# Optimization experiments

Hardware: AMD Instinct MI355X
Metric: run time of the kernel (lower is better)

The kernel has to match this reference:

```python
import jax, jax.numpy as jnp
import numpy as np

B, T, S, E = 32, 32, 8, 512
H, D, FF, NL = 8, 64, 2048, 4
AEMB, NACT = 64, 18
L = T * S            # qlen = 256
MEM = 256
KLEN = L + MEM       # 512


def _ln(x, g, b, eps=1e-5):
    m = jnp.mean(x, -1, keepdims=True)
    v = jnp.mean(jnp.square(x - m), -1, keepdims=True)
    return (x - m) * jax.lax.rsqrt(v + eps) * g + b


def _rel_shift(bd):
    # bd: [qlen, klen, B, H] -- TransformerXL rel-shift trick
    q, k, b, h = bd.shape
    bd = jnp.pad(bd, ((0, 0), (1, 0), (0, 0), (0, 0)))
    return bd.reshape(k + 1, q, b, h)[1:].reshape(q, k, b, h)


def setup_inputs() -> dict:
    key = jax.random.key(0)
    ks = jax.random.split(key, 20)
    s = 0.02  # weight init scale
    x = jax.random.normal(ks[0], (B, T, S, E), jnp.float32)
    action = jax.random.randint(ks[1], (B, T), 0, NACT, dtype=jnp.int32)
    i = jnp.arange(L)[:, None]
    j = jnp.arange(KLEN)[None, :]
    attn_mask = j > (i + MEM)                      # True = masked (causal w/ memory)
    positions = jnp.arange(KLEN - 1, -1, -1, dtype=jnp.int32)  # TXL descending positions
    mems = jax.random.normal(ks[2], (NL, MEM, B, E), jnp.float32) * 0.1
    return {
        'x': x, 'action': action, 'attn_mask': attn_mask, 'positions': positions,
        'mems': mems,
        'act_emb': jax.random.normal(ks[3], (NACT, AEMB), jnp.float32) * s,
        'stem_w1': jax.random.normal(ks[4], (E + AEMB, E), jnp.float32) * s,
        'stem_ln1_g': jnp.ones((E,), jnp.float32), 'stem_ln1_b': jnp.zeros((E,), jnp.float32),
        'stem_w2': jax.random.normal(ks[5], (E, E), jnp.float32) * s,
        'stem_ln2_g': jnp.ones((E,), jnp.float32), 'stem_ln2_b': jnp.zeros((E,), jnp.float32),
        'lnf_g': jnp.ones((E,), jnp.float32), 'lnf_b': jnp.zeros((E,), jnp.float32),
        'u_bias': jax.random.normal(ks[6], (H, D), jnp.float32) * s,
        'v_bias': jax.random.normal(ks[7], (H, D), jnp.float32) * s,
        'Wqkv': jax.random.normal(ks[8], (NL, E, 3 * H * D), jnp.float32) * s,
        'Wr': jax.random.normal(ks[9], (NL, E, H * D), jnp.float32) * s,
        'Wo': jax.random.normal(ks[10], (NL, H * D, E), jnp.float32) * s,
        'ln1_g': jnp.ones((NL, E), jnp.float32), 'ln1_b': jnp.zeros((NL, E), jnp.float32),
        'W1': jax.random.normal(ks[11], (NL, E, FF), jnp.float32) * s,
        'b1': jnp.zeros((NL, FF), jnp.float32),
        'W2': jax.random.normal(ks[12], (NL, FF, E), jnp.float32) * s,
        'b2': jnp.zeros((NL, E), jnp.float32),
        'ln2_g': jnp.ones((NL, E), jnp.float32), 'ln2_b': jnp.zeros((NL, E), jnp.float32),
    }


def reference(x, action, attn_mask, positions, mems, act_emb,
              stem_w1, stem_ln1_g, stem_ln1_b, stem_w2, stem_ln2_g, stem_ln2_b,
              lnf_g, lnf_b, u_bias, v_bias, Wqkv, Wr, Wo,
              ln1_g, ln1_b, W1, b1, W2, b2, ln2_g, ln2_b):
    Bv, Tv, Sv, Ev = x.shape
    Hh, Dd = u_bias.shape
    qlen = Tv * Sv
    # --- stem (StateMixer, concat type) ---
    xs = x.reshape(Bv, qlen, Ev).transpose(1, 0, 2)                # [L,B,E] time-major
    a = act_emb[action]                                            # [B,T,AEMB]
    a = jnp.repeat(a, Sv, axis=1).transpose(1, 0, 2)               # [L,B,AEMB]
    h = jnp.concatenate([xs, a], -1) @ stem_w1
    h = jax.nn.relu(_ln(h, stem_ln1_g, stem_ln1_b))
    h = _ln(h @ stem_w2, stem_ln2_g, stem_ln2_b)
    feats = _ln(h, lnf_g, lnf_b, eps=1e-6)
    # --- sinusoidal positional encoding of relative positions ---
    pf = positions.astype(jnp.float32)
    inv = 1.0 / (10000.0 ** (jnp.arange(0, Ev, 2, dtype=jnp.float32) / Ev))
    ang = pf[:, None] * inv[None, :]
    pos_emb = jnp.concatenate([jnp.sin(ang), jnp.cos(ang)], -1)    # [KLEN,E]
    scale = 1.0 / np.sqrt(Dd)
    out = feats
    for l in range(Wqkv.shape[0]):
        cat = jnp.concatenate([mems[l], out], 0)                   # [klen,B,E]
        klen = cat.shape[0]
        q, k, v = jnp.split(cat @ Wqkv[l], 3, -1)
        q = q[-qlen:].reshape(qlen, Bv, Hh, Dd)
        k = k.reshape(klen, Bv, Hh, Dd)
        v = v.reshape(klen, Bv, Hh, Dd)
        r = (pos_emb @ Wr[l]).reshape(klen, Hh, Dd)
        AC = jnp.einsum('ibhd,jbhd->ijbh', q + u_bias, k)
        BD = _rel_shift(jnp.einsum('ibhd,jhd->ijbh', q + v_bias, r))
        score = (AC + BD) * scale
        score = jnp.where(attn_mask[:, :, None, None], jnp.float32(-1e30), score)
        attn = jax.nn.softmax(score, axis=1)
        ao = jnp.einsum('ijbh,jbhd->ibhd', attn, v).reshape(qlen, Bv, Hh * Dd) @ Wo[l]
        h1 = _ln(out + ao, ln1_g[l], ln1_b[l])
        ff = jax.nn.relu(h1 @ W1[l] + b1[l]) @ W2[l] + b2[l]
        out = _ln(h1 + ff, ln2_g[l], ln2_b[l])
    return out.transpose(1, 0, 2).reshape(Bv, Tv, Sv, Ev)
```

## Files before the change

### kernel.cpp

```cpp
#include <hip/hip_runtime.h>


typedef __attribute__((ext_vector_type(8))) short bf8_t;
typedef __attribute__((ext_vector_type(4))) float f4_t;
typedef __attribute__((ext_vector_type(16))) float fx16;

__device__ __forceinline__ ushort f2bf(float f) {
    uint u = __float_as_uint(f);
    u += 0x7FFFu + ((u >> 16) & 1u);
    return (ushort)(u >> 16);
}
__device__ __forceinline__ float b2f(ushort h) {
    return __uint_as_float(((uint)h) << 16);
}
__device__ __forceinline__ void gload16(const void* g, void* l) {
    __builtin_amdgcn_global_load_lds((const __attribute__((address_space(1))) void*)g,
                                     (__attribute__((address_space(3))) void*)l, 16, 0, 0);
}

__device__ __forceinline__ void mma32_step(const ushort* __restrict__ As,
                                           const ushort* __restrict__ Bs,
                                           int rowA0, int colB0,
                                           int l31, int hi, fx16 acc[2][2])
{
#pragma unroll
    for (int kk = 0; kk < 4; ++kk) {
        bf8_t av[2], bv[2];
#pragma unroll
        for (int i = 0; i < 2; ++i) {
            const int row = rowA0 + i * 32 + l31;
            const int ch = (kk * 2 + hi) ^ (row & 7);
            av[i] = *(const bf8_t*)(As + row * 64 + ch * 8);
        }
#pragma unroll
        for (int j = 0; j < 2; ++j) {
            const int row = colB0 + j * 32 + l31;
            const int ch = (kk * 2 + hi) ^ (row & 7);
            bv[j] = *(const bf8_t*)(Bs + row * 64 + ch * 8);
        }
#pragma unroll
        for (int i = 0; i < 2; ++i)
#pragma unroll
            for (int j = 0; j < 2; ++j)
                acc[i][j] = __builtin_amdgcn_mfma_f32_32x32x16_bf16(av[i], bv[j], acc[i][j], 0, 0, 0);
    }
}

template<bool BIAS, bool RELU, bool OUTBF>
__global__ __launch_bounds__(256)
void gemm_bf(const ushort* __restrict__ A, int lda,
             const ushort* __restrict__ Bt, int ldb,
             const float* __restrict__ bias,
             void* __restrict__ Cp, int ldc,
             int M, int N, int K)
{
    __shared__ __align__(16) ushort sh[17408];
    ushort* As = sh;
    ushort* Bs = sh + 8192;
    const int t = threadIdx.x;
    const int w = t >> 6, lane = t & 63;
    const int wr = w >> 1, wc = w & 1;
    const int l31 = lane & 31, hi = lane >> 5;
    const int m0 = blockIdx.y * 128, n0 = blockIdx.x * 128;

    const int srow = w * 8 + (lane >> 3);
    const int gchunk = (lane & 7) ^ (srow & 7);
    const ushort* Ag = A + (size_t)(m0 + srow) * lda + gchunk * 8;
    const ushort* Bg = Bt + (size_t)(n0 + srow) * ldb + gchunk * 8;
    ushort* Asw = As + w * 512;
    ushort* Bsw = Bs + w * 512;

    fx16 acc[2][2];
#pragma unroll
    for (int i = 0; i < 2; ++i)
#pragma unroll
        for (int j = 0; j < 2; ++j)
#pragma unroll
            for (int r = 0; r < 16; ++r) acc[i][j][r] = 0.f;

    for (int k0 = 0; k0 < K; k0 += 64) {
#pragma unroll
        for (int c = 0; c < 4; ++c) {
            gload16(Ag + (size_t)c * 32 * lda, Asw + c * 2048);
            gload16(Bg + (size_t)c * 32 * ldb, Bsw + c * 2048);
        }
        Ag += 64; Bg += 64;
        __syncthreads();
        mma32_step(As, Bs, wr * 64, wc * 64, l31, hi, acc);
        __syncthreads();
    }
    const int crow0 = wr * 64, ccol0 = wc * 64;
    if (OUTBF) {
        ushort* Cs = sh;
#pragma unroll
        for (int i = 0; i < 2; ++i)
#pragma unroll
            for (int j = 0; j < 2; ++j) {
                const int colb = ccol0 + j * 32 + l31;
                float bb = BIAS ? bias[n0 + colb] : 0.f;
                fx16 v = acc[i][j];
#pragma unroll
                for (int r = 0; r < 16; ++r) {
                    float o = v[r] + bb;
                    if (RELU) o = fmaxf(o, 0.f);
                    const int rw = crow0 + i * 32 + (r & 3) + 8 * (r >> 2) + 4 * hi;
                    Cs[rw * 136 + colb] = f2bf(o);
                }
            }
        __syncthreads();
        const int orow = t >> 1, oc0 = (t & 1) * 64;
        ushort* dst = (ushort*)Cp + (size_t)(m0 + orow) * ldc + n0 + oc0;
#pragma unroll
        for (int u = 0; u < 8; ++u)
            *(bf8_t*)(dst + u * 8) = *(const bf8_t*)(Cs + orow * 136 + oc0 + u * 8);
    } else {
        float* C = (float*)Cp;
#pragma unroll
        for (int i = 0; i < 2; ++i)
#pragma unroll
            for (int j = 0; j < 2; ++j) {
                const int colb = n0 + ccol0 + j * 32 + l31;
                float bb = BIAS ? bias[colb] : 0.f;
                fx16 v = acc[i][j];
#pragma unroll
                for (int r = 0; r < 16; ++r) {
                    float o = v[r] + bb;
                    if (RELU) o = fmaxf(o, 0.f);
                    const int rw = crow0 + i * 32 + (r & 3) + 8 * (r >> 2) + 4 * hi;
                    C[(size_t)(m0 + rw) * ldc + colb] = o;
                }
            }
    }
}

__global__ __launch_bounds__(256)
void gemm_qkv(const ushort* __restrict__ A, const ushort* __restrict__ Bt,
              ushort* __restrict__ qout, ushort* __restrict__ kvout)
{
    __shared__ __align__(16) ushort sh[17408];
    ushort* As = sh;
    ushort* Bs = sh + 8192;
    const int t = threadIdx.x;
    const int w = t >> 6, lane = t & 63;
    const int wr = w >> 1, wc = w & 1;
    const int l31 = lane & 31, hi = lane >> 5;
    const int m0 = blockIdx.y * 128, n0 = blockIdx.x * 128;

    const int srow = w * 8 + (lane >> 3);
    const int gchunk = (lane & 7) ^ (srow & 7);
    const ushort* Ag = A + (size_t)(m0 + srow) * 512 + gchunk * 8;
    const ushort* Bg = Bt + (size_t)(n0 + srow) * 512 + gchunk * 8;
    ushort* Asw = As + w * 512;
    ushort* Bsw = Bs + w * 512;

    fx16 acc[2][2];
#pragma unroll
    for (int i = 0; i < 2; ++i)
#pragma unroll
        for (int j = 0; j < 2; ++j)
#pragma unroll
            for (int r = 0; r < 16; ++r) acc[i][j][r] = 0.f;

    for (int k0 = 0; k0 < 512; k0 += 64) {
#pragma unroll
        for (int c = 0; c < 4; ++c) {
            gload16(Ag + (size_t)c * 32 * 512, Asw + c * 2048);
            gload16(Bg + (size_t)c * 32 * 512, Bsw + c * 2048);
        }
        Ag += 64; Bg += 64;
        __syncthreads();
        mma32_step(As, Bs, wr * 64, wc * 64, l31, hi, acc);
        __syncthreads();
    }
    const int crow0 = wr * 64, ccol0 = wc * 64;
    ushort* Cs = sh;
#pragma unroll
    for (int i = 0; i < 2; ++i)
#pragma unroll
        for (int j = 0; j < 2; ++j) {
            const int colb = ccol0 + j * 32 + l31;
            fx16 v = acc[i][j];
#pragma unroll
            for (int r = 0; r < 16; ++r) {
                const int rw = crow0 + i * 32 + (r & 3) + 8 * (r >> 2) + 4 * hi;
                Cs[rw * 136 + colb] = f2bf(v[r]);
            }
        }
    __syncthreads();
    ushort* base; size_t ldc2;
    if (n0 < 512) { base = qout + n0; ldc2 = 512; }
    else          { base = kvout + (size_t)8192 * 1024 + (n0 - 512); ldc2 = 1024; }
    const int orow = t >> 1, oc0 = (t & 1) * 64;
    ushort* dst = base + (size_t)(m0 + orow) * ldc2 + oc0;
#pragma unroll
    for (int u = 0; u < 8; ++u)
        *(bf8_t*)(dst + u * 8) = *(const bf8_t*)(Cs + orow * 136 + oc0 + u * 8);
}

template<bool BIAS>
__global__ __launch_bounds__(256)
void gemm_sk(const ushort* __restrict__ A, int lda,
             const ushort* __restrict__ Bt, int ldb,
             const float* __restrict__ bias,
             float* __restrict__ C0, float* __restrict__ C1, int ldc, int KH)
{
    __shared__ __align__(16) ushort sh[16384];
    ushort* As = sh;
    ushort* Bs = sh + 8192;
    const int t = threadIdx.x;
    const int w = t >> 6, lane = t & 63;
    const int wr = w >> 1, wc = w & 1;
    const int l31 = lane & 31, hi = lane >> 5;
    const int m0 = blockIdx.y * 128, n0 = blockIdx.x * 128;
    const int z = blockIdx.z;
    A += (size_t)z * KH; Bt += (size_t)z * KH;
    float* C = z ? C1 : C0;

    const int srow = w * 8 + (lane >> 3);
    const int gchunk = (lane & 7) ^ (srow & 7);
    const ushort* Ag = A + (size_t)(m0 + srow) * lda + gchunk * 8;
    const ushort* Bg = Bt + (size_t)(n0 + srow) * ldb + gchunk * 8;
    ushort* Asw = As + w * 512;
    ushort* Bsw = Bs + w * 512;

    fx16 acc[2][2];
#pragma unroll
    for (int i = 0; i < 2; ++i)
#pragma unroll
        for (int j = 0; j < 2; ++j)
#pragma unroll
            for (int r = 0; r < 16; ++r) acc[i][j][r] = 0.f;

    for (int k0 = 0; k0 < KH; k0 += 64) {
#pragma unroll
        for (int c = 0; c < 4; ++c) {
            gload16(Ag + (size_t)c * 32 * lda, Asw + c * 2048);
            gload16(Bg + (size_t)c * 32 * ldb, Bsw + c * 2048);
        }
        Ag += 64; Bg += 64;
        __syncthreads();
        mma32_step(As, Bs, wr * 64, wc * 64, l31, hi, acc);
        __syncthreads();
    }
    const int crow0 = wr * 64, ccol0 = wc * 64;
#pragma unroll
    for (int i = 0; i < 2; ++i)
#pragma unroll
        for (int j = 0; j < 2; ++j) {
            const int colb = n0 + ccol0 + j * 32 + l31;
            float bb = (BIAS && z == 0) ? bias[colb] : 0.f;
            fx16 v = acc[i][j];
#pragma unroll
            for (int r = 0; r < 16; ++r) {
                const int rw = crow0 + i * 32 + (r & 3) + 8 * (r >> 2) + 4 * hi;
                C[(size_t)(m0 + rw) * ldc + colb] = v[r] + bb;
            }
        }
}

template<int RMODE, bool TROUT>
__global__ __launch_bounds__(256)
void ln_k(const float* __restrict__ X, const float* __restrict__ X2,
          const void* __restrict__ Rp,
          const float* __restrict__ g, const float* __restrict__ bt,
          float* __restrict__ Yf, ushort* __restrict__ Yb,
          float eps, int do_relu)
{
    const int row  = blockIdx.x * 4 + (threadIdx.x >> 6);
    const int lane = threadIdx.x & 63;
    const float* xp = X + (size_t)row * 512 + lane * 8;
    float4 x0 = *(const float4*)xp, x1 = *(const float4*)(xp + 4);
    float v[8] = {x0.x, x0.y, x0.z, x0.w, x1.x, x1.y, x1.z, x1.w};
    if (RMODE == 3 || RMODE == 4) {
        const float* p2 = X2 + (size_t)row * 512 + lane * 8;
        float4 a0 = *(const float4*)p2, a1 = *(const float4*)(p2 + 4);
        v[0] += a0.x; v[1] += a0.y; v[2] += a0.z; v[3] += a0.w;
        v[4] += a1.x; v[5] += a1.y; v[6] += a1.z; v[7] += a1.w;
    }
    if (RMODE == 1 || RMODE == 4) {
        const float* rp = (const float*)Rp + (size_t)row * 512 + lane * 8;
        float4 r0 = *(const float4*)rp, r1 = *(const float4*)(rp + 4);
        v[0] += r0.x; v[1] += r0.y; v[2] += r0.z; v[3] += r0.w;
        v[4] += r1.x; v[5] += r1.y; v[6] += r1.z; v[7] += r1.w;
    } else if (RMODE == 2 || RMODE == 3) {
        const ushort* rp = (const ushort*)Rp + (size_t)row * 512 + lane * 8;
        ushort4 r0 = *(const ushort4*)rp, r1 = *(const ushort4*)(rp + 4);
        v[0] += b2f(r0.x); v[1] += b2f(r0.y); v[2] += b2f(r0.z); v[3] += b2f(r0.w);
        v[4] += b2f(r1.x); v[5] += b2f(r1.y); v[6] += b2f(r1.z); v[7] += b2f(r1.w);
    }
    float s = 0.f;
#pragma unroll
    for (int i = 0; i < 8; ++i) s += v[i];
#pragma unroll
    for (int m = 1; m < 64; m <<= 1) s += __shfl_xor(s, m);
    float mean = s * (1.f / 512.f);
    float q = 0.f;
#pragma unroll
    for (int i = 0; i < 8; ++i) { float d = v[i] - mean; q = fmaf(d, d, q); }
#pragma unroll
    for (int m = 1; m < 64; m <<= 1) q += __shfl_xor(q, m);
    float rstd = rsqrtf(q * (1.f / 512.f) + eps);
    float4 g0 = *(const float4*)(g + lane * 8), g1 = *(const float4*)(g + lane * 8 + 4);
    float4 c0 = *(const float4*)(bt + lane * 8), c1 = *(const float4*)(bt + lane * 8 + 4);
    float gv[8] = {g0.x, g0.y, g0.z, g0.w, g1.x, g1.y, g1.z, g1.w};
    float bv[8] = {c0.x, c0.y, c0.z, c0.w, c1.x, c1.y, c1.z, c1.w};
    float o[8];
#pragma unroll
    for (int i = 0; i < 8; ++i) {
        o[i] = (v[i] - mean) * rstd * gv[i] + bv[i];
        if (do_relu) o[i] = fmaxf(o[i], 0.f);
    }
    if (Yf) {
        float* yp;
        if (TROUT) {
            const int bq = row & 31, lq = row >> 5;
            yp = Yf + ((size_t)bq * 256 + lq) * 512 + lane * 8;
        } else {
            yp = Yf + (size_t)row * 512 + lane * 8;
        }
        *(float4*)yp       = make_float4(o[0], o[1], o[2], o[3]);
        *(float4*)(yp + 4) = make_float4(o[4], o[5], o[6], o[7]);
    }
    if (Yb) {
        ushort* yp = Yb + (size_t)row * 512 + lane * 8;
        ushort4 w0, w1;
        w0.x = f2bf(o[0]); w0.y = f2bf(o[1]); w0.z = f2bf(o[2]); w0.w = f2bf(o[3]);
        w1.x = f2bf(o[4]); w1.y = f2bf(o[5]); w1.z = f2bf(o[6]); w1.w = f2bf(o[7]);
        *(ushort4*)yp       = w0;
        *(ushort4*)(yp + 4) = w1;
    }
}

__global__ __launch_bounds__(256)
void ln_stem2(const float* __restrict__ X,
              const float* __restrict__ g1, const float* __restrict__ b1,
              const float* __restrict__ g2, const float* __restrict__ b2,
              float* __restrict__ Yf, ushort* __restrict__ Yb)
{
    const int row  = blockIdx.x * 4 + (threadIdx.x >> 6);
    const int lane = threadIdx.x & 63;
    const float* xp = X + (size_t)row * 512 + lane * 8;
    float4 x0 = *(const float4*)xp, x1 = *(const float4*)(xp + 4);
    float v[8] = {x0.x, x0.y, x0.z, x0.w, x1.x, x1.y, x1.z, x1.w};
    float s = 0.f;
#pragma unroll
    for (int i = 0; i < 8; ++i) s += v[i];
#pragma unroll
    for (int m = 1; m < 64; m <<= 1) s += __shfl_xor(s, m);
    float mean = s * (1.f / 512.f);
    float q = 0.f;
#pragma unroll
    for (int i = 0; i < 8; ++i) { float d = v[i] - mean; q = fmaf(d, d, q); }
#pragma unroll
    for (int m = 1; m < 64; m <<= 1) q += __shfl_xor(q, m);
    float rstd = rsqrtf(q * (1.f / 512.f) + 1e-5f);
#pragma unroll
    for (int i = 0; i < 8; ++i)
        v[i] = (v[i] - mean) * rstd * g1[lane * 8 + i] + b1[lane * 8 + i];
    s = 0.f;
#pragma unroll
    for (int i = 0; i < 8; ++i) s += v[i];
#pragma unroll
    for (int m = 1; m < 64; m <<= 1) s += __shfl_xor(s, m);
    mean = s * (1.f / 512.f);
    q = 0.f;
#pragma unroll
    for (int i = 0; i < 8; ++i) { float d = v[i] - mean; q = fmaf(d, d, q); }
#pragma unroll
    for (int m = 1; m < 64; m <<= 1) q += __shfl_xor(q, m);
    rstd = rsqrtf(q * (1.f / 512.f) + 1e-6f);
    float o[8];
#pragma unroll
    for (int i = 0; i < 8; ++i)
        o[i] = (v[i] - mean) * rstd * g2[lane * 8 + i] + b2[lane * 8 + i];
    float* yp = Yf + (size_t)row * 512 + lane * 8;
    *(float4*)yp       = make_float4(o[0], o[1], o[2], o[3]);
    *(float4*)(yp + 4) = make_float4(o[4], o[5], o[6], o[7]);
    ushort* yb = Yb + (size_t)row * 512 + lane * 8;
    ushort4 w0, w1;
    w0.x = f2bf(o[0]); w0.y = f2bf(o[1]); w0.z = f2bf(o[2]); w0.w = f2bf(o[3]);
    w1.x = f2bf(o[4]); w1.y = f2bf(o[5]); w1.z = f2bf(o[6]); w1.w = f2bf(o[7]);
    *(ushort4*)yb       = w0;
    *(ushort4*)(yb + 4) = w1;
}

__global__ __launch_bounds__(256)
void wtrans(const float* __restrict__ in, ushort* __restrict__ out, int K, int N)
{
    __shared__ float tl[32][33];
    const size_t bo = (size_t)blockIdx.z * K * N;
    in += bo; out += bo;
    const int k0 = blockIdx.y * 32, n0 = blockIdx.x * 32;
    const int tx = threadIdx.x & 31, ty = threadIdx.x >> 5;
    for (int i = ty; i < 32; i += 8) tl[i][tx] = in[(size_t)(k0 + i) * N + n0 + tx];
    __syncthreads();
    for (int i = ty; i < 32; i += 8) out[(size_t)(n0 + i) * K + k0 + tx] = f2bf(tl[tx][i]);
}

__global__ void convk(const float* __restrict__ in, ushort* __restrict__ out)
{
    int i = (blockIdx.x * 256 + threadIdx.x) * 4;
    float4 v = *(const float4*)(in + i);
    ushort4 o;
    o.x = f2bf(v.x); o.y = f2bf(v.y); o.z = f2bf(v.z); o.w = f2bf(v.w);
    *(ushort4*)(out + i) = o;
}

__global__ void build_xcat(const float* __restrict__ x, const int* __restrict__ action,
                           const float* __restrict__ act_emb, ushort* __restrict__ xcat)
{
    int idx = blockIdx.x * 256 + threadIdx.x;
    int n = idx / 576, e = idx - n * 576;
    int l = n >> 5, b = n & 31;
    float v;
    if (e < 512) v = x[((size_t)b * 256 + l) * 512 + e];
    else         v = act_emb[action[b * 32 + (l >> 3)] * 64 + (e - 512)];
    xcat[idx] = f2bf(v);
}

__global__ void build_posemb(ushort* __restrict__ pe)
{
    int idx = blockIdx.x * 256 + threadIdx.x;
    int j = idx >> 9, c = idx & 511;
    float pf = (float)(511 - j);
    int i2 = (c < 256) ? c : c - 256;
    float inv = expf(-(float)i2 * 0.03597789207803197f);
    float ang = pf * inv;
    pe[idx] = f2bf((c < 256) ? sinf(ang) : cosf(ang));
}

__global__ __launch_bounds__(512)
void attn_mfma(const ushort* __restrict__ q,
               const ushort* __restrict__ kv,
               const ushort* __restrict__ rb,
               const float* __restrict__ ub, const float* __restrict__ vb,
               ushort* __restrict__ ao)
{
    __shared__ __align__(16) ushort Ks[64][72];
    __shared__ __align__(16) ushort Vs[64][72];
    __shared__ __align__(16) ushort Rs[192][72];
    __shared__ __align__(16) ushort Ps[8][16][72];
    const int t = threadIdx.x;
    const int wv = t >> 6, lane = t & 63;
    const int lc = lane & 15, lr = lane >> 4;
    const int bh = (int)blockIdx.x >> 1, ihalf = blockIdx.x & 1;
    const int b = bh >> 3, h = bh & 7;
    const int i0 = ihalf << 7;
    const int iw = i0 + wv * 16;

    bf8_t au[2], aw[2];
#pragma unroll
    for (int kk = 0; kk < 2; ++kk) {
        const ushort* qp = q + ((size_t)(iw + lc) * 32 + b) * 512 + h * 64 + kk * 32 + lr * 8;
        bf8_t q8 = *(const bf8_t*)qp;
        const float* up = ub + h * 64 + kk * 32 + lr * 8;
        const float* vp = vb + h * 64 + kk * 32 + lr * 8;
#pragma unroll
        for (int e = 0; e < 8; ++e) {
            float qf = b2f((ushort)q8[e]);
            au[kk][e] = (short)f2bf(qf + up[e]);
            aw[kk][e] = (short)f2bf(qf + vp[e]);
        }
    }

    const int jl = t >> 3, d0 = (t & 7) * 8;
    const int vrow = ((t >> 3) & 7) * 8 + wv;

    f4_t o[4];
#pragma unroll
    for (int d = 0; d < 4; ++d) o[d] = (f4_t){0.f, 0.f, 0.f, 0.f};
    float mrun[4] = {-3.0e38f, -3.0e38f, -3.0e38f, -3.0e38f};
    float lrun[4] = {0.f, 0.f, 0.f, 0.f};

    {
        *(bf8_t*)&Ks[jl][d0] = *(const bf8_t*)(kv + ((size_t)jl * 32 + b) * 1024 + h * 64 + d0);
        bf8_t vv = *(const bf8_t*)(kv + ((size_t)vrow * 32 + b) * 1024 + 512 + h * 64 + d0);
#pragma unroll
        for (int e = 0; e < 8; ++e) Vs[d0 + e][vrow] = (ushort)vv[e];
        const int rbase0 = 128 - i0;
#pragma unroll
        for (int p = 0; p < 3; ++p) {
            const int jr = min(rbase0 + p * 64 + jl, 511);
            *(bf8_t*)&Rs[p * 64 + jl][d0] = *(const bf8_t*)(rb + (size_t)jr * 512 + h * 64 + d0);
        }
    }
    __syncthreads();

    const int njt = ihalf ? 8 : 6;
    for (int jt = 0; jt < njt; ++jt) {
        const int j0 = jt << 6;
        bf8_t pk, pv, pr;
        const bool pfq = (jt + 1 < njt);
        if (pfq) {
            const int j0n = j0 + 64;
            pk = *(const bf8_t*)(kv + ((size_t)(j0n + jl) * 32 + b) * 1024 + h * 64 + d0);
            pv = *(const bf8_t*)(kv + ((size_t)(j0n + vrow) * 32 + b) * 1024 + 512 + h * 64 + d0);
            const int jr = min(j0n - i0 + 256 + jl, 511);
            pr = *(const bf8_t*)(rb + (size_t)jr * 512 + h * 64 + d0);
        }
        if (j0 <= iw + 271) {
            f4_t acf[4], bdf[5];
#pragma unroll
            for (int jj = 0; jj < 4; ++jj) acf[jj] = (f4_t){0.f, 0.f, 0.f, 0.f};
#pragma unroll
            for (int fj = 0; fj < 5; ++fj) bdf[fj] = (f4_t){0.f, 0.f, 0.f, 0.f};
#pragma unroll
            for (int jj = 0; jj < 4; ++jj)
#pragma unroll
                for (int kk = 0; kk < 2; ++kk) {
                    bf8_t kf = *(const bf8_t*)&Ks[jj * 16 + lc][kk * 32 + lr * 8];
                    acf[jj] = __builtin_amdgcn_mfma_f32_16x16x32_bf16(au[kk], kf, acf[jj], 0, 0, 0);
                }
            const int rboff = 112 - wv * 16;
#pragma unroll
            for (int fj = 0; fj < 5; ++fj) {
                const int lbase = rboff + fj * 16;
                const int prow = ((jt + (lbase >> 6)) % 3) * 64 + (lbase & 63) + lc;
#pragma unroll
                for (int kk = 0; kk < 2; ++kk) {
                    bf8_t rf = *(const bf8_t*)&Rs[prow][kk * 32 + lr * 8];
                    bdf[fj] = __builtin_amdgcn_mfma_f32_16x16x32_bf16(aw[kk], rf, bdf[fj], 0, 0, 0);
                }
            }
            float pm[4][4];
            float mt[4] = {-3.0e38f, -3.0e38f, -3.0e38f, -3.0e38f};
            const int jbase = j0 + lc - iw - 256;
#pragma unroll
            for (int rg = 0; rg < 4; ++rg) {
                const int il = lr * 4 + rg;
                const int srcl = (lane & 48) | ((lc + 15 - il) & 15);
                float shf[5];
#pragma unroll
                for (int fj = 0; fj < 5; ++fj) shf[fj] = __shfl(bdf[fj][rg], srcl, 64);
#pragma unroll
                for (int jj = 0; jj < 4; ++jj) {
                    float bd = (lc > il) ? shf[jj + 1] : shf[jj];
                    float s = (acf[jj][rg] + bd) * 0.125f;
                    if (jbase + jj * 16 > il) s = -1e30f;
                    pm[jj][rg] = s;
                    mt[rg] = fmaxf(mt[rg], s);
                }
            }
            float corr[4];
#pragma unroll
            for (int rg = 0; rg < 4; ++rg) {
#pragma unroll
                for (int mm = 1; mm < 16; mm <<= 1)
                    mt[rg] = fmaxf(mt[rg], __shfl_xor(mt[rg], mm, 64));
                float mnew = fmaxf(mrun[rg], mt[rg]);
                corr[rg] = __expf(mrun[rg] - mnew);
                mrun[rg] = mnew;
            }
            float ps4[4] = {0.f, 0.f, 0.f, 0.f};
#pragma unroll
            for (int jj = 0; jj < 4; ++jj)
#pragma unroll
                for (int rg = 0; rg < 4; ++rg) {
                    float p = __expf(pm[jj][rg] - mrun[rg]);
                    ps4[rg] += p;
                    Ps[wv][lr * 4 + rg][jj * 16 + lc] = f2bf(p);
                }
#pragma unroll
            for (int rg = 0; rg < 4; ++rg) {
#pragma unroll
                for (int mm = 1; mm < 16; mm <<= 1)
                    ps4[rg] += __shfl_xor(ps4[rg], mm, 64);
                lrun[rg] = lrun[rg] * corr[rg] + ps4[rg];
            }
            float c0 = __shfl(corr[0], (lc >> 2) << 4, 64);
            float c1 = __shfl(corr[1], (lc >> 2) << 4, 64);
            float c2 = __shfl(corr[2], (lc >> 2) << 4, 64);
            float c3 = __shfl(corr[3], (lc >> 2) << 4, 64);
            float myc = (lc & 2) ? ((lc & 1) ? c3 : c2) : ((lc & 1) ? c1 : c0);
#pragma unroll
            for (int db = 0; db < 4; ++db)
#pragma unroll
                for (int rg = 0; rg < 4; ++rg) o[db][rg] *= myc;
#pragma unroll
            for (int kb = 0; kb < 2; ++kb) {
                bf8_t pf = *(const bf8_t*)&Ps[wv][lc][kb * 32 + lr * 8];
#pragma unroll
                for (int db = 0; db < 4; ++db) {
                    bf8_t vf = *(const bf8_t*)&Vs[db * 16 + lc][kb * 32 + lr * 8];
                    o[db] = __builtin_amdgcn_mfma_f32_16x16x32_bf16(vf, pf, o[db], 0, 0, 0);
                }
            }
        }
        __syncthreads();
        if (pfq) {
            *(bf8_t*)&Ks[jl][d0] = pk;
#pragma unroll
            for (int e = 0; e < 8; ++e) Vs[d0 + e][vrow] = (ushort)pv[e];
            const int phys = (jt % 3) * 64 + jl;
            *(bf8_t*)&Rs[phys][d0] = pr;
        }
        __syncthreads();
    }
    float i4[4];
#pragma unroll
    for (int rg = 0; rg < 4; ++rg) i4[rg] = 1.f / lrun[rg];
    float s0 = __shfl(i4[0], (lc >> 2) << 4, 64);
    float s1 = __shfl(i4[1], (lc >> 2) << 4, 64);
    float s2 = __shfl(i4[2], (lc >> 2) << 4, 64);
    float s3 = __shfl(i4[3], (lc >> 2) << 4, 64);
    float myi = (lc & 2) ? ((lc & 1) ? s3 : s2) : ((lc & 1) ? s1 : s0);
#pragma unroll
    for (int db = 0; db < 4; ++db)
#pragma unroll
        for (int rg = 0; rg < 4; ++rg)
            Ps[wv][lc][db * 16 + lr * 4 + rg] = f2bf(o[db][rg] * myi);
    const int il2 = lane >> 2, dsg = (lane & 3) << 4;
    bf8_t e0 = *(const bf8_t*)&Ps[wv][il2][dsg];
    bf8_t e1 = *(const bf8_t*)&Ps[wv][il2][dsg + 8];
    ushort* dst = ao + ((size_t)(iw + il2) * 32 + b) * 512 + h * 64 + dsg;
    *(bf8_t*)dst = e0;
    *(bf8_t*)(dst + 8) = e1;
}

extern "C" void kernel_launch(void* const* d_in, const int* in_sizes, int n_in,
                              void* d_out, int out_size, void* d_ws, size_t ws_size,
                              hipStream_t stream)
{
    const float* x       = (const float*)d_in[0];
    const int*   action  = (const int*)d_in[1];
    const float* mems    = (const float*)d_in[4];
    const float* act_emb = (const float*)d_in[5];
    const float* stem_w1 = (const float*)d_in[6];
    const float* sln1g   = (const float*)d_in[7];
    const float* sln1b   = (const float*)d_in[8];
    const float* stem_w2 = (const float*)d_in[9];
    const float* sln2g   = (const float*)d_in[10];
    const float* sln2b   = (const float*)d_in[11];
    const float* lnfg    = (const float*)d_in[12];
    const float* lnfb    = (const float*)d_in[13];
    const float* ub      = (const float*)d_in[14];
    const float* vb      = (const float*)d_in[15];
    const float* Wqkv    = (const float*)d_in[16];
    const float* Wr      = (const float*)d_in[17];
    const float* Wo      = (const float*)d_in[18];
    const float* ln1g    = (const float*)d_in[19];
    const float* ln1b    = (const float*)d_in[20];
    const float* W1      = (const float*)d_in[21];
    const float* b1      = (const float*)d_in[22];
    const float* W2      = (const float*)d_in[23];
    const float* b2      = (const float*)d_in[24];
    const float* ln2g    = (const float*)d_in[25];
    const float* ln2b    = (const float*)d_in[26];
    float* out = (float*)d_out;

    char* W = (char*)d_ws;
    float*  cur32 = (float*) (W + 0);
    float*  g32   = (float*) (W + 16777216);
    ushort* curb  = (ushort*)(W + 33554432);
    ushort* h1b   = (ushort*)(W + 41943040);
    ushort* qb    = (ushort*)(W + 50331648);
    ushort* kvb   = (ushort*)(W + 58720256);
    ushort* rbuf  = (ushort*)(W + 92274688);
    ushort* peb   = (ushort*)(W + 92798976);
    ushort* wts   = (ushort*)(W + 93323264);
    ushort* xcatb = kvb;
    ushort* ff1b  = kvb;
    float*  wopart = (float*)kvb;
    ushort* memsb = (ushort*)g32;
    ushort* w1t    = wts;
    ushort* w2t    = wts + 294912;
    ushort* wqkvT  = wts + 557056;
    ushort* wrT    = wts + 3702784;
    ushort* woT    = wts + 4751360;
    ushort* w1T    = wts + 5799936;
    ushort* w2T    = wts + 9994240;

    dim3 blk(256);
    wtrans<<<dim3(16, 18, 1), blk, 0, stream>>>(stem_w1, w1t, 576, 512);
    wtrans<<<dim3(16, 16, 1), blk, 0, stream>>>(stem_w2, w2t, 512, 512);
    wtrans<<<dim3(48, 16, 4), blk, 0, stream>>>(Wqkv, wqkvT, 512, 1536);
    wtrans<<<dim3(16, 16, 4), blk, 0, stream>>>(Wr, wrT, 512, 512);
    wtrans<<<dim3(16, 16, 4), blk, 0, stream>>>(Wo, woT, 512, 512);
    wtrans<<<dim3(64, 16, 4), blk, 0, stream>>>(W1, w1T, 512, 2048);
    wtrans<<<dim3(16, 64, 4), blk, 0, stream>>>(W2, w2T, 2048, 512);
    build_posemb<<<1024, blk, 0, stream>>>(peb);

    build_xcat<<<18432, blk, 0, stream>>>(x, action, act_emb, xcatb);
    gemm_bf<false, false, false><<<dim3(4, 64), blk, 0, stream>>>(xcatb, 576, w1t, 576, nullptr, g32, 512, 8192, 512, 576);
    ln_k<0, false><<<2048, blk, 0, stream>>>(g32, nullptr, nullptr, sln1g, sln1b, nullptr, curb, 1e-5f, 1);
    gemm_bf<false, false, false><<<dim3(4, 64), blk, 0, stream>>>(curb, 512, w2t, 512, nullptr, g32, 512, 8192, 512, 512);
    ln_stem2<<<2048, blk, 0, stream>>>(g32, sln2g, sln2b, lnfg, lnfb, cur32, curb);

    for (int l = 0; l < 4; ++l) {
        const ushort* wqkvT_l = wqkvT + (size_t)l * 786432;
        convk<<<4096, blk, 0, stream>>>(mems + (size_t)l * 4194304, memsb);
        gemm_qkv<<<dim3(12, 64), blk, 0, stream>>>(curb, wqkvT_l, qb, kvb);
        gemm_bf<false, false, true><<<dim3(8, 64), blk, 0, stream>>>(memsb, 512, wqkvT_l + 262144, 512, nullptr, kvb, 1024, 8192, 1024, 512);
        gemm_bf<false, false, true><<<dim3(4, 4), blk, 0, stream>>>(peb, 512, wrT + (size_t)l * 262144, 512, nullptr, rbuf, 512, 512, 512, 512);
        attn_mfma<<<512, dim3(512), 0, stream>>>(qb, kvb, rbuf, ub, vb, h1b);
        gemm_sk<false><<<dim3(4, 64, 2), blk, 0, stream>>>(h1b, 512, woT + (size_t)l * 262144, 512, nullptr, g32, wopart, 512, 256);
        ln_k<4, false><<<2048, blk, 0, stream>>>(g32, wopart, cur32, ln1g + l * 512, ln1b + l * 512, nullptr, h1b, 1e-5f, 0);
        gemm_bf<true, true, true><<<dim3(16, 64), blk, 0, stream>>>(h1b, 512, w1T + (size_t)l * 1048576, 512, b1 + l * 2048, ff1b, 2048, 8192, 2048, 512);
        gemm_sk<true><<<dim3(4, 64, 2), blk, 0, stream>>>(ff1b, 2048, w2T + (size_t)l * 1048576, 2048, b2 + l * 512, g32, cur32, 512, 1024);
        if (l == 3)
            ln_k<3, true><<<2048, blk, 0, stream>>>(g32, cur32, h1b, ln2g + l * 512, ln2b + l * 512, out, nullptr, 1e-5f, 0);
        else
            ln_k<3, false><<<2048, blk, 0, stream>>>(g32, cur32, h1b, ln2g + l * 512, ln2b + l * 512, cur32, curb, 1e-5f, 0);
    }
}
```

Measured before the change: 909.2 us.

## Double-buffer GEMM LDS tiles with K-step 32 to overlap loads and MFMA

The three bf16 MFMA GEMM kernels move from a single 64-wide K tile loaded and consumed between two barriers to two 32-wide K buffers in LDS. The next tile is prefetched with global_load_lds while the current one feeds the MFMAs, leaving one barrier per step. The aim is to hide global-memory latency behind compute. In exchange there are twice as many loop iterations and barriers, a narrower 4-chunk XOR swizzle that may raise LDS bank conflicts, and a reliance on the single barrier giving correct ordering for the asynchronous LDS loads.

```diff
diff --git a/kernel.cpp b/kernel.cpp
--- a/kernel.cpp
+++ b/kernel.cpp
@@ -18,25 +18,25 @@
                                      (__attribute__((address_space(3))) void*)l, 16, 0, 0);
 }
 
-__device__ __forceinline__ void mma32_step(const ushort* __restrict__ As,
-                                           const ushort* __restrict__ Bs,
-                                           int rowA0, int colB0,
-                                           int l31, int hi, fx16 acc[2][2])
-{
-#pragma unroll
-    for (int kk = 0; kk < 4; ++kk) {
+__device__ __forceinline__ void mma32_k32(const ushort* __restrict__ As,
+                                          const ushort* __restrict__ Bs,
+                                          int rowA0, int colB0,
+                                          int l31, int hi, fx16 acc[2][2])
+{
+#pragma unroll
+    for (int kk = 0; kk < 2; ++kk) {
         bf8_t av[2], bv[2];
 #pragma unroll
         for (int i = 0; i < 2; ++i) {
             const int row = rowA0 + i * 32 + l31;
-            const int ch = (kk * 2 + hi) ^ (row & 7);
-            av[i] = *(const bf8_t*)(As + row * 64 + ch * 8);
+            const int ch = (kk * 2 + hi) ^ (row & 3);
+            av[i] = *(const bf8_t*)(As + row * 32 + ch * 8);
         }
 #pragma unroll
         for (int j = 0; j < 2; ++j) {
             const int row = colB0 + j * 32 + l31;
-            const int ch = (kk * 2 + hi) ^ (row & 7);
-            bv[j] = *(const bf8_t*)(Bs + row * 64 + ch * 8);
+            const int ch = (kk * 2 + hi) ^ (row & 3);
+            bv[j] = *(const bf8_t*)(Bs + row * 32 + ch * 8);
         }
 #pragma unroll
         for (int i = 0; i < 2; ++i)
@@ -55,20 +55,22 @@
              int M, int N, int K)
 {
     __shared__ __align__(16) ushort sh[17408];
-    ushort* As = sh;
-    ushort* Bs = sh + 8192;
+    ushort* A0 = sh;
+    ushort* A1 = sh + 4096;
+    ushort* B0 = sh + 8192;
+    ushort* B1 = sh + 12288;
     const int t = threadIdx.x;
     const int w = t >> 6, lane = t & 63;
     const int wr = w >> 1, wc = w & 1;
     const int l31 = lane & 31, hi = lane >> 5;
     const int m0 = blockIdx.y * 128, n0 = blockIdx.x * 128;
 
-    const int srow = w * 8 + (lane >> 3);
-    const int gchunk = (lane & 7) ^ (srow & 7);
-    const ushort* Ag = A + (size_t)(m0 + srow) * lda + gchunk * 8;
-    const ushort* Bg = Bt + (size_t)(n0 + srow) * ldb + gchunk * 8;
-    ushort* Asw = As + w * 512;
-    ushort* Bsw = Bs + w * 512;
+    const int srow = t >> 2;
+    const int gch = (t & 3) ^ (srow & 3);
+    const ushort* Ag = A + (size_t)(m0 + srow) * lda + gch * 8;
+    const ushort* Bg = Bt + (size_t)(n0 + srow) * ldb + gch * 8;
+    ushort* dA0 = A0 + w * 512;  ushort* dA1 = A1 + w * 512;
+    ushort* dB0 = B0 + w * 512;  ushort* dB1 = B1 + w * 512;
 
     fx16 acc[2][2];
 #pragma unroll
@@ -78,15 +80,25 @@
 #pragma unroll
             for (int r = 0; r < 16; ++r) acc[i][j][r] = 0.f;
 
-    for (int k0 = 0; k0 < K; k0 += 64) {
-#pragma unroll
-        for (int c = 0; c < 4; ++c) {
-            gload16(Ag + (size_t)c * 32 * lda, Asw + c * 2048);
-            gload16(Bg + (size_t)c * 32 * ldb, Bsw + c * 2048);
-        }
-        Ag += 64; Bg += 64;
-        __syncthreads();
-        mma32_step(As, Bs, wr * 64, wc * 64, l31, hi, acc);
+    gload16(Ag,            dA0);
+    gload16(Ag + 64 * lda, dA0 + 2048);
+    gload16(Bg,            dB0);
+    gload16(Bg + 64 * ldb, dB0 + 2048);
+    __syncthreads();
+
+    for (int k0 = 0; k0 < K; k0 += 32) {
+        const bool odd = (k0 & 32) != 0;
+        const ushort* Ac = odd ? A1 : A0;
+        const ushort* Bc = odd ? B1 : B0;
+        if (k0 + 32 < K) {
+            const ushort* Agn = Ag + k0 + 32;
+            const ushort* Bgn = Bg + k0 + 32;
+            gload16(Agn,            odd ? dA0 : dA1);
+            gload16(Agn + 64 * lda, (odd ? dA0 : dA1) + 2048);
+            gload16(Bgn,            odd ? dB0 : dB1);
+            gload16(Bgn + 64 * ldb, (odd ? dB0 : dB1) + 2048);
+        }
+        mma32_k32(Ac, Bc, wr * 64, wc * 64, l31, hi, acc);
         __syncthreads();
     }
     const int crow0 = wr * 64, ccol0 = wc * 64;
@@ -138,20 +150,22 @@
               ushort* __restrict__ qout, ushort* __restrict__ kvout)
 {
     __shared__ __align__(16) ushort sh[17408];
-    ushort* As = sh;
-    ushort* Bs = sh + 8192;
+    ushort* A0 = sh;
+    ushort* A1 = sh + 4096;
+    ushort* B0 = sh + 8192;
+    ushort* B1 = sh + 12288;
     const int t = threadIdx.x;
     const int w = t >> 6, lane = t & 63;
     const int wr = w >> 1, wc = w & 1;
     const int l31 = lane & 31, hi = lane >> 5;
     const int m0 = blockIdx.y * 128, n0 = blockIdx.x * 128;
 
-    const int srow = w * 8 + (lane >> 3);
-    const int gchunk = (lane & 7) ^ (srow & 7);
-    const ushort* Ag = A + (size_t)(m0 + srow) * 512 + gchunk * 8;
-    const ushort* Bg = Bt + (size_t)(n0 + srow) * 512 + gchunk * 8;
-    ushort* Asw = As + w * 512;
-    ushort* Bsw = Bs + w * 512;
+    const int srow = t >> 2;
+    const int gch = (t & 3) ^ (srow & 3);
+    const ushort* Ag = A + (size_t)(m0 + srow) * 512 + gch * 8;
+    const ushort* Bg = Bt + (size_t)(n0 + srow) * 512 + gch * 8;
+    ushort* dA0 = A0 + w * 512;  ushort* dA1 = A1 + w * 512;
+    ushort* dB0 = B0 + w * 512;  ushort* dB1 = B1 + w * 512;
 
     fx16 acc[2][2];
 #pragma unroll
@@ -161,15 +175,25 @@
 #pragma unroll
             for (int r = 0; r < 16; ++r) acc[i][j][r] = 0.f;
 
-    for (int k0 = 0; k0 < 512; k0 += 64) {
-#pragma unroll
-        for (int c = 0; c < 4; ++c) {
-            gload16(Ag + (size_t)c * 32 * 512, Asw + c * 2048);
-            gload16(Bg + (size_t)c * 32 * 512, Bsw + c * 2048);
-        }
-        Ag += 64; Bg += 64;
-        __syncthreads();
-        mma32_step(As, Bs, wr * 64, wc * 64, l31, hi, acc);
+    gload16(Ag,            dA0);
+    gload16(Ag + 64 * 512, dA0 + 2048);
+    gload16(Bg,            dB0);
+    gload16(Bg + 64 * 512, dB0 + 2048);
+    __syncthreads();
+
+    for (int k0 = 0; k0 < 512; k0 += 32) {
+        const bool odd = (k0 & 32) != 0;
+        const ushort* Ac = odd ? A1 : A0;
+        const ushort* Bc = odd ? B1 : B0;
+        if (k0 + 32 < 512) {
+            const ushort* Agn = Ag + k0 + 32;
+            const ushort* Bgn = Bg + k0 + 32;
+            gload16(Agn,            odd ? dA0 : dA1);
+            gload16(Agn + 64 * 512, (odd ? dA0 : dA1) + 2048);
+            gload16(Bgn,            odd ? dB0 : dB1);
+            gload16(Bgn + 64 * 512, (odd ? dB0 : dB1) + 2048);
+        }
+        mma32_k32(Ac, Bc, wr * 64, wc * 64, l31, hi, acc);
         __syncthreads();
     }
     const int crow0 = wr * 64, ccol0 = wc * 64;
@@ -205,8 +229,10 @@
              float* __restrict__ C0, float* __restrict__ C1, int ldc, int KH)
 {
     __shared__ __align__(16) ushort sh[16384];
-    ushort* As = sh;
-    ushort* Bs = sh + 8192;
+    ushort* A0 = sh;
+    ushort* A1 = sh + 4096;
+    ushort* B0 = sh + 8192;
+    ushort* B1 = sh + 12288;
     const int t = threadIdx.x;
     const int w = t >> 6, lane = t & 63;
     const int wr = w >> 1, wc = w & 1;
@@ -216,12 +242,12 @@
     A += (size_t)z * KH; Bt += (size_t)z * KH;
     float* C = z ? C1 : C0;
 
-    const int srow = w * 8 + (lane >> 3);
-    const int gchunk = (lane & 7) ^ (srow & 7);
-    const ushort* Ag = A + (size_t)(m0 + srow) * lda + gchunk * 8;
-    const ushort* Bg = Bt + (size_t)(n0 + srow) * ldb + gchunk * 8;
-    ushort* Asw = As + w * 512;
-    ushort* Bsw = Bs + w * 512;
+    const int srow = t >> 2;
+    const int gch = (t & 3) ^ (srow & 3);
+    const ushort* Ag = A + (size_t)(m0 + srow) * lda + gch * 8;
+    const ushort* Bg = Bt + (size_t)(n0 + srow) * ldb + gch * 8;
+    ushort* dA0 = A0 + w * 512;  ushort* dA1 = A1 + w * 512;
+    ushort* dB0 = B0 + w * 512;  ushort* dB1 = B1 + w * 512;
 
     fx16 acc[2][2];
 #pragma unroll
@@ -231,15 +257,25 @@
 #pragma unroll
             for (int r = 0; r < 16; ++r) acc[i][j][r] = 0.f;
 
-    for (int k0 = 0; k0 < KH; k0 += 64) {
-#pragma unroll
-        for (int c = 0; c < 4; ++c) {
-            gload16(Ag + (size_t)c * 32 * lda, Asw + c * 2048);
-            gload16(Bg + (size_t)c * 32 * ldb, Bsw + c * 2048);
-        }
-        Ag += 64; Bg += 64;
-        __syncthreads();
-        mma32_step(As, Bs, wr * 64, wc * 64, l31, hi, acc);
+    gload16(Ag,            dA0);
+    gload16(Ag + 64 * lda, dA0 + 2048);
+    gload16(Bg,            dB0);
+    gload16(Bg + 64 * ldb, dB0 + 2048);
+    __syncthreads();
+
+    for (int k0 = 0; k0 < KH; k0 += 32) {
+        const bool odd = (k0 & 32) != 0;
+        const ushort* Ac = odd ? A1 : A0;
+        const ushort* Bc = odd ? B1 : B0;
+        if (k0 + 32 < KH) {
+            const ushort* Agn = Ag + k0 + 32;
+            const ushort* Bgn = Bg + k0 + 32;
+            gload16(Agn,            odd ? dA0 : dA1);
+            gload16(Agn + 64 * lda, (odd ? dA0 : dA1) + 2048);
+            gload16(Bgn,            odd ? dB0 : dB1);
+            gload16(Bgn + 64 * ldb, (odd ? dB0 : dB1) + 2048);
+        }
+        mma32_k32(Ac, Bc, wr * 64, wc * 64, l31, hi, acc);
         __syncthreads();
     }
     const int crow0 = wr * 64, ccol0 = wc * 64;
```

After: 960.1 us. +5.6%, slower.
